# Kernel optimization log

Hardware: AMD Instinct MI355X
Metric: run time of the kernel (lower is better)

Reference implementation:

```python
import jax, jax.numpy as jnp
import numpy as np

N, M, DX, DY, H = 1024, 1024, 64, 16, 128
EPS = 1e-07


def setup_inputs() -> dict:
    key = jax.random.key(0)
    ks = jax.random.split(key, 9)
    din = DX + DY
    # Inputs
    X = jax.random.normal(ks[0], (N, DX), dtype=jnp.float32)
    U = jax.random.normal(ks[1], (M, DY), dtype=jnp.float32)
    Y = jax.random.normal(ks[2], (N, DY), dtype=jnp.float32)
    # MLP params (Linear(din,H), Softplus, Linear(H,H), Softplus, Linear(H,1))
    W1 = jax.random.normal(ks[3], (din, H), dtype=jnp.float32) / np.sqrt(din)
    b1 = jax.random.normal(ks[4], (H,), dtype=jnp.float32) * 0.01
    W2 = jax.random.normal(ks[5], (H, H), dtype=jnp.float32) / np.sqrt(H)
    b2 = jax.random.normal(ks[6], (H,), dtype=jnp.float32) * 0.01
    W3 = jax.random.normal(ks[7], (H, 1), dtype=jnp.float32) / np.sqrt(H)
    b3 = jax.random.normal(ks[8], (1,), dtype=jnp.float32) * 0.01
    return {"X_tensor": X, "U_tensor": U, "Y_tensor": Y,
            "W1": W1, "b1": b1, "W2": W2, "b2": b2, "W3": W3, "b3": b3}


def reference(X_tensor, U_tensor, Y_tensor, W1, b1, W2, b2, W3, b3):
    # phi_potential_network evaluated on every (x_i, u_j) pair.
    # Instead of materializing the [n, m, d_x + d_y] concatenation, split the
    # first linear layer: cat(x, u) @ W1 == x @ W1[:DX] + u @ W1[DX:]  (same math).
    hx = jnp.einsum('nd,dh->nh', X_tensor, W1[:DX])        # [n, H]
    hu = jnp.einsum('md,dh->mh', U_tensor, W1[DX:])        # [m, H]
    h = jax.nn.softplus(hx[:, None, :] + hu[None, :, :] + b1)   # [n, m, H]
    h = jax.nn.softplus(jnp.einsum('nmh,hk->nmk', h, W2) + b2)  # [n, m, H]
    phi_vals = jnp.einsum('nmh,hk->nmk', h, W3)[..., 0] + b3[0]  # [n, m]
    # entropic OT dual slackness + stable log-mean-exp over dual samples
    cost_matrix = Y_tensor @ U_tensor.T                     # [n, m]
    slackness = (cost_matrix - phi_vals) / EPS
    log_mean_exp = (jax.nn.logsumexp(slackness, axis=1, keepdims=True)
                    - jnp.log(jnp.float32(M)))
    psi_estimate = EPS * log_mean_exp                       # [n, 1]
    return psi_estimate
```

## Files before the change

kernel.cpp:

```cpp
#include <hip/hip_runtime.h>
#include <hip/hip_bf16.h>

#define NN 1024
#define MM 1024
#define DX 64
#define DY 16
#define HH 128

#define EPSF   1e-7f
#define LOG2E  1.4426950408889634f
#define LN2    0.6931471805599453f
#define K2     14426950.408889634f
#define LNM    6.9314718055994531f

typedef __bf16          bf16x8_t __attribute__((ext_vector_type(8)));
typedef float           f32x4_t  __attribute__((ext_vector_type(4)));
typedef unsigned short  u16x8_t  __attribute__((ext_vector_type(8)));

__device__ __forceinline__ unsigned short f2bf(float f) {
    unsigned int u = __float_as_uint(f);
    u += 0x7fffu + ((u >> 16) & 1u);
    return (unsigned short)(u >> 16);
}

__device__ __forceinline__ float sp(float x) {
    float t = __builtin_amdgcn_exp2f(x * LOG2E);
    return LN2 * __builtin_amdgcn_logf(1.0f + t);
}

__global__ void prep(const float* __restrict__ X, const float* __restrict__ U,
                     const float* __restrict__ Y, const float* __restrict__ W1,
                     const float* __restrict__ b1, const float* __restrict__ W2,
                     float* __restrict__ hx, float* __restrict__ hu,
                     unsigned short* __restrict__ w2t, float* __restrict__ costT)
{
    const int blk = blockIdx.x, tid = threadIdx.x;
    if (blk < NN) {
        const int n = blk, h = tid;
        float acc = b1[h];
        #pragma unroll 8
        for (int d = 0; d < DX; ++d) acc += X[n*DX+d] * W1[d*HH+h];
        hx[n*HH+h] = acc;
    } else if (blk < NN+MM) {
        const int m = blk - NN, h = tid;
        float acc = 0.f;
        #pragma unroll
        for (int d = 0; d < DY; ++d) acc += U[m*DY+d] * W1[(DX+d)*HH+h];
        hu[m*HH+h] = acc;
    } else if (blk < NN+MM+HH) {
        const int c = blk - (NN+MM), k = tid;
        w2t[c*HH+k] = f2bf(W2[k*HH+c]);
    } else {
        const int m = blk - (NN+MM+HH);
        float u[DY];
        #pragma unroll
        for (int d = 0; d < DY; ++d) u[d] = U[m*DY+d];
        #pragma unroll
        for (int r = 0; r < NN/128; ++r) {
            const int n = tid + r*128;
            float acc = 0.f;
            #pragma unroll
            for (int d = 0; d < DY; ++d) acc += Y[n*DY+d] * u[d];
            costT[m*NN+n] = acc;
        }
    }
}

__global__ __launch_bounds__(256, 2) void
otmain(const float* __restrict__ hx, const float* __restrict__ hu,
       const unsigned short* __restrict__ w2t,
       const float* __restrict__ b2, const float* __restrict__ W3,
       const float* __restrict__ b3, const float* __restrict__ costT,
       float* __restrict__ out)
{
    __shared__ unsigned short w2s[HH*HH];
    __shared__ float red[4][2][2];

    const int tid  = threadIdx.x;
    const int lane = tid & 63;
    const int w    = tid >> 6;
    const int nb   = blockIdx.x * 2;

    #pragma unroll
    for (int it = 0; it < 8; ++it) {
        const int chunk = tid + it*256;
        const int lin   = chunk << 4;
        const int c     = lin >> 8;
        const int swz   = lin ^ ((c & 7) << 4);
        *reinterpret_cast<u16x8_t*>(reinterpret_cast<char*>(w2s) + swz) =
            *reinterpret_cast<const u16x8_t*>(reinterpret_cast<const char*>(w2t) + lin);
    }

    const int il = lane & 1;
    const int jl = (lane >> 1) & 7;
    const int g  = lane >> 4;
    const int cl = lane & 15;

    float hxv[4][8];
    #pragma unroll
    for (int ks = 0; ks < 4; ++ks) {
        const float4 p0 = *reinterpret_cast<const float4*>(&hx[(nb+il)*HH + ks*32 + g*8]);
        const float4 p1 = *reinterpret_cast<const float4*>(&hx[(nb+il)*HH + ks*32 + g*8 + 4]);
        hxv[ks][0]=p0.x; hxv[ks][1]=p0.y; hxv[ks][2]=p0.z; hxv[ks][3]=p0.w;
        hxv[ks][4]=p1.x; hxv[ks][5]=p1.y; hxv[ks][6]=p1.z; hxv[ks][7]=p1.w;
    }
    float b2v[8], w3v[8];
    #pragma unroll
    for (int nt = 0; nt < 8; ++nt) { b2v[nt] = b2[nt*16+cl]; w3v[nt] = W3[nt*16+cl]; }
    const float b3v = b3[0];

    float mx[4], sv[4];
    #pragma unroll
    for (int q = 0; q < 4; ++q) { mx[q] = -3.0e38f; sv[q] = 0.f; }

    __syncthreads();

    for (int cch = 0; cch < 16; ++cch) {
        const int mb = cch * 64;
        const int m0 = mb + 16*w + jl;
        const int m1 = m0 + 8;
        f32x4_t acc0[8], acc1[8];
        #pragma unroll
        for (int nt = 0; nt < 8; ++nt)
            #pragma unroll
            for (int q = 0; q < 4; ++q) { acc0[nt][q] = 0.f; acc1[nt][q] = 0.f; }

        #pragma unroll
        for (int ks = 0; ks < 4; ++ks) {
            const int kf = ks*32 + g*8;
            const float4 u0a = *reinterpret_cast<const float4*>(&hu[m0*HH + kf]);
            const float4 u0b = *reinterpret_cast<const float4*>(&hu[m0*HH + kf + 4]);
            const float4 u1a = *reinterpret_cast<const float4*>(&hu[m1*HH + kf]);
            const float4 u1b = *reinterpret_cast<const float4*>(&hu[m1*HH + kf + 4]);
            u16x8_t a0u, a1u;
            a0u[0]=f2bf(sp(hxv[ks][0]+u0a.x)); a0u[1]=f2bf(sp(hxv[ks][1]+u0a.y));
            a0u[2]=f2bf(sp(hxv[ks][2]+u0a.z)); a0u[3]=f2bf(sp(hxv[ks][3]+u0a.w));
            a0u[4]=f2bf(sp(hxv[ks][4]+u0b.x)); a0u[5]=f2bf(sp(hxv[ks][5]+u0b.y));
            a0u[6]=f2bf(sp(hxv[ks][6]+u0b.z)); a0u[7]=f2bf(sp(hxv[ks][7]+u0b.w));
            a1u[0]=f2bf(sp(hxv[ks][0]+u1a.x)); a1u[1]=f2bf(sp(hxv[ks][1]+u1a.y));
            a1u[2]=f2bf(sp(hxv[ks][2]+u1a.z)); a1u[3]=f2bf(sp(hxv[ks][3]+u1a.w));
            a1u[4]=f2bf(sp(hxv[ks][4]+u1b.x)); a1u[5]=f2bf(sp(hxv[ks][5]+u1b.y));
            a1u[6]=f2bf(sp(hxv[ks][6]+u1b.z)); a1u[7]=f2bf(sp(hxv[ks][7]+u1b.w));
            const bf16x8_t a0 = __builtin_bit_cast(bf16x8_t, a0u);
            const bf16x8_t a1 = __builtin_bit_cast(bf16x8_t, a1u);

            #pragma unroll
            for (int nt = 0; nt < 8; ++nt) {
                const int cidx = nt*16 + cl;
                const int off  = (cidx*256 + ks*64 + g*16) ^ ((cidx & 7) << 4);
                const bf16x8_t bfr = *reinterpret_cast<const bf16x8_t*>(
                        reinterpret_cast<const char*>(w2s) + off);
                acc0[nt] = __builtin_amdgcn_mfma_f32_16x16x32_bf16(a0, bfr, acc0[nt], 0, 0, 0);
                acc1[nt] = __builtin_amdgcn_mfma_f32_16x16x32_bf16(a1, bfr, acc1[nt], 0, 0, 0);
            }
        }

        #pragma unroll
        for (int t = 0; t < 2; ++t) {
            float phi0=0.f, phi1=0.f, phi2=0.f, phi3=0.f;
            #pragma unroll
            for (int nt = 0; nt < 8; ++nt) {
                const f32x4_t a = t ? acc1[nt] : acc0[nt];
                phi0 += sp(a[0] + b2v[nt]) * w3v[nt];
                phi1 += sp(a[1] + b2v[nt]) * w3v[nt];
                phi2 += sp(a[2] + b2v[nt]) * w3v[nt];
                phi3 += sp(a[3] + b2v[nt]) * w3v[nt];
            }
            #pragma unroll
            for (int st = 1; st < 16; st <<= 1) {
                phi0 += __shfl_xor(phi0, st, 64);
                phi1 += __shfl_xor(phi1, st, 64);
                phi2 += __shfl_xor(phi2, st, 64);
                phi3 += __shfl_xor(phi3, st, 64);
            }
            const int jm = mb + 16*w + 8*t + 2*g;
            const float2 cA = *reinterpret_cast<const float2*>(&costT[jm*NN + nb]);
            const float2 cB = *reinterpret_cast<const float2*>(&costT[(jm+1)*NN + nb]);
            const float dv0 = cA.x - (phi0 + b3v);
            const float dv1 = cA.y - (phi1 + b3v);
            const float dv2 = cB.x - (phi2 + b3v);
            const float dv3 = cB.y - (phi3 + b3v);
            #define UPD(q, d) { const float mo = mx[q]; const float mn = fmaxf(mo, (d)); \
                sv[q] = sv[q]*__builtin_amdgcn_exp2f(K2*(mo-mn)) \
                      + __builtin_amdgcn_exp2f(K2*((d)-mn)); mx[q] = mn; }
            UPD(0, dv0) UPD(1, dv1) UPD(2, dv2) UPD(3, dv3)
            #undef UPD
        }
    }

    float fmx[2], fs[2];
    #pragma unroll
    for (int i = 0; i < 2; ++i) {
        const float m1v = mx[i], m2v = mx[i+2];
        const float Mv  = fmaxf(m1v, m2v);
        fmx[i] = Mv;
        fs[i]  = sv[i]  *__builtin_amdgcn_exp2f(K2*(m1v-Mv))
               + sv[i+2]*__builtin_amdgcn_exp2f(K2*(m2v-Mv));
    }
    if (cl != 0) { fs[0] = 0.f; fs[1] = 0.f; }
    #pragma unroll
    for (int st = 1; st < 64; st <<= 1) {
        #pragma unroll
        for (int i = 0; i < 2; ++i) {
            const float om = __shfl_xor(fmx[i], st, 64);
            const float os = __shfl_xor(fs[i],  st, 64);
            const float Mv = fmaxf(fmx[i], om);
            fs[i]  = fs[i]*__builtin_amdgcn_exp2f(K2*(fmx[i]-Mv))
                   + os  *__builtin_amdgcn_exp2f(K2*(om-Mv));
            fmx[i] = Mv;
        }
    }
    if (lane == 0) {
        red[w][0][0] = fmx[0]; red[w][0][1] = fs[0];
        red[w][1][0] = fmx[1]; red[w][1][1] = fs[1];
    }
    __syncthreads();
    if (tid < 2) {
        float Mv = red[0][tid][0], Sv = red[0][tid][1];
        #pragma unroll
        for (int ww = 1; ww < 4; ++ww) {
            const float om = red[ww][tid][0], os = red[ww][tid][1];
            const float M2 = fmaxf(Mv, om);
            Sv = Sv*__builtin_amdgcn_exp2f(K2*(Mv-M2))
               + os*__builtin_amdgcn_exp2f(K2*(om-M2));
            Mv = M2;
        }
        out[nb + tid] = Mv + EPSF*(LN2*__builtin_amdgcn_logf(Sv) - LNM);
    }
}

extern "C" void kernel_launch(void* const* d_in, const int* in_sizes, int n_in,
                              void* d_out, int out_size, void* d_ws, size_t ws_size,
                              hipStream_t stream)
{
    const float* X  = (const float*)d_in[0];
    const float* U  = (const float*)d_in[1];
    const float* Y  = (const float*)d_in[2];
    const float* W1 = (const float*)d_in[3];
    const float* b1 = (const float*)d_in[4];
    const float* W2 = (const float*)d_in[5];
    const float* b2 = (const float*)d_in[6];
    const float* W3 = (const float*)d_in[7];
    const float* b3 = (const float*)d_in[8];
    float* out = (float*)d_out;

    char* ws = (char*)d_ws;
    float*          hx    = (float*)(ws);
    float*          hu    = (float*)(ws + 524288);
    unsigned short* w2t   = (unsigned short*)(ws + 1048576);
    float*          costT = (float*)(ws + 1081344);

    prep<<<dim3(3200), dim3(128), 0, stream>>>(X, U, Y, W1, b1, W2, hx, hu, w2t, costT);
    otmain<<<dim3(512), dim3(256), 0, stream>>>(hx, hu, w2t, b2, W3, b3, costT, out);
}
```

Before: 206.4 us.

## Split m-range across two blocks per row pair, fold softplus constants, add merge kernel

The main kernel now launches twice as many blocks, each handling half of the m range, and writes partial (max, sum) pairs that a new merge kernel combines into the final log-mean-exp. The LOG2E/LN2 factors of softplus are folded into hx, hu, b2 and W3 in prep, and the online logsumexp update now uses a single exp2 per element. Launch bounds are raised to 4 blocks per CU, and the cost matrix is stored n-major so reads follow m. This is meant to fill more CUs and cut transcendental and multiply work, at the cost of an extra kernel launch, a workspace round-trip, and register pressure under the tighter launch bound.

After: 411.8 us. 2x slower.

```diff
diff --git a/kernel.cpp b/kernel.cpp
--- a/kernel.cpp
+++ b/kernel.cpp
@@ -23,16 +23,15 @@
     return (unsigned short)(u >> 16);
 }
 
-__device__ __forceinline__ float sp(float x) {
-    float t = __builtin_amdgcn_exp2f(x * LOG2E);
-    return LN2 * __builtin_amdgcn_logf(1.0f + t);
+__device__ __forceinline__ float l2e1(float s) {
+    return __builtin_amdgcn_logf(1.0f + __builtin_amdgcn_exp2f(s));
 }
 
 __global__ void prep(const float* __restrict__ X, const float* __restrict__ U,
                      const float* __restrict__ Y, const float* __restrict__ W1,
                      const float* __restrict__ b1, const float* __restrict__ W2,
                      float* __restrict__ hx, float* __restrict__ hu,
-                     unsigned short* __restrict__ w2t, float* __restrict__ costT)
+                     unsigned short* __restrict__ w2t, float* __restrict__ costN)
 {
     const int blk = blockIdx.x, tid = threadIdx.x;
     if (blk < NN) {
@@ -40,38 +39,38 @@
         float acc = b1[h];
         #pragma unroll 8
         for (int d = 0; d < DX; ++d) acc += X[n*DX+d] * W1[d*HH+h];
-        hx[n*HH+h] = acc;
+        hx[n*HH+h] = acc * LOG2E;
     } else if (blk < NN+MM) {
         const int m = blk - NN, h = tid;
         float acc = 0.f;
         #pragma unroll
         for (int d = 0; d < DY; ++d) acc += U[m*DY+d] * W1[(DX+d)*HH+h];
-        hu[m*HH+h] = acc;
+        hu[m*HH+h] = acc * LOG2E;
     } else if (blk < NN+MM+HH) {
         const int c = blk - (NN+MM), k = tid;
         w2t[c*HH+k] = f2bf(W2[k*HH+c]);
     } else {
-        const int m = blk - (NN+MM+HH);
-        float u[DY];
-        #pragma unroll
-        for (int d = 0; d < DY; ++d) u[d] = U[m*DY+d];
-        #pragma unroll
-        for (int r = 0; r < NN/128; ++r) {
-            const int n = tid + r*128;
+        const int n = blk - (NN+MM+HH);
+        float yv[DY];
+        #pragma unroll
+        for (int d = 0; d < DY; ++d) yv[d] = Y[n*DY+d];
+        #pragma unroll
+        for (int r = 0; r < MM/128; ++r) {
+            const int m = tid + r*128;
             float acc = 0.f;
             #pragma unroll
-            for (int d = 0; d < DY; ++d) acc += Y[n*DY+d] * u[d];
-            costT[m*NN+n] = acc;
-        }
-    }
-}
-
-__global__ __launch_bounds__(256, 2) void
+            for (int d = 0; d < DY; ++d) acc += U[m*DY+d] * yv[d];
+            costN[n*MM+m] = acc;
+        }
+    }
+}
+
+__global__ __launch_bounds__(256, 4) void
 otmain(const float* __restrict__ hx, const float* __restrict__ hu,
        const unsigned short* __restrict__ w2t,
        const float* __restrict__ b2, const float* __restrict__ W3,
-       const float* __restrict__ b3, const float* __restrict__ costT,
-       float* __restrict__ out)
+       const float* __restrict__ b3, const float* __restrict__ costN,
+       float2* __restrict__ part)
 {
     __shared__ unsigned short w2s[HH*HH];
     __shared__ float red[4][2][2];
@@ -79,7 +78,8 @@
     const int tid  = threadIdx.x;
     const int lane = tid & 63;
     const int w    = tid >> 6;
-    const int nb   = blockIdx.x * 2;
+    const int nb   = (blockIdx.x >> 1) * 2;
+    const int half = blockIdx.x & 1;
 
     #pragma unroll
     for (int it = 0; it < 8; ++it) {
@@ -106,7 +106,10 @@
     }
     float b2v[8], w3v[8];
     #pragma unroll
-    for (int nt = 0; nt < 8; ++nt) { b2v[nt] = b2[nt*16+cl]; w3v[nt] = W3[nt*16+cl]; }
+    for (int nt = 0; nt < 8; ++nt) {
+        b2v[nt] = b2[nt*16+cl] * LOG2E;
+        w3v[nt] = W3[nt*16+cl] * LN2;
+    }
     const float b3v = b3[0];
 
     float mx[4], sv[4];
@@ -115,8 +118,8 @@
 
     __syncthreads();
 
-    for (int cch = 0; cch < 16; ++cch) {
-        const int mb = cch * 64;
+    for (int cc = 0; cc < 8; ++cc) {
+        const int mb = (half*8 + cc) * 64;
         const int m0 = mb + 16*w + jl;
         const int m1 = m0 + 8;
         f32x4_t acc0[8], acc1[8];
@@ -132,17 +135,15 @@
             const float4 u0b = *reinterpret_cast<const float4*>(&hu[m0*HH + kf + 4]);
             const float4 u1a = *reinterpret_cast<const float4*>(&hu[m1*HH + kf]);
             const float4 u1b = *reinterpret_cast<const float4*>(&hu[m1*HH + kf + 4]);
-            u16x8_t a0u, a1u;
-            a0u[0]=f2bf(sp(hxv[ks][0]+u0a.x)); a0u[1]=f2bf(sp(hxv[ks][1]+u0a.y));
-            a0u[2]=f2bf(sp(hxv[ks][2]+u0a.z)); a0u[3]=f2bf(sp(hxv[ks][3]+u0a.w));
-            a0u[4]=f2bf(sp(hxv[ks][4]+u0b.x)); a0u[5]=f2bf(sp(hxv[ks][5]+u0b.y));
-            a0u[6]=f2bf(sp(hxv[ks][6]+u0b.z)); a0u[7]=f2bf(sp(hxv[ks][7]+u0b.w));
-            a1u[0]=f2bf(sp(hxv[ks][0]+u1a.x)); a1u[1]=f2bf(sp(hxv[ks][1]+u1a.y));
-            a1u[2]=f2bf(sp(hxv[ks][2]+u1a.z)); a1u[3]=f2bf(sp(hxv[ks][3]+u1a.w));
-            a1u[4]=f2bf(sp(hxv[ks][4]+u1b.x)); a1u[5]=f2bf(sp(hxv[ks][5]+u1b.y));
-            a1u[6]=f2bf(sp(hxv[ks][6]+u1b.z)); a1u[7]=f2bf(sp(hxv[ks][7]+u1b.w));
-            const bf16x8_t a0 = __builtin_bit_cast(bf16x8_t, a0u);
-            const bf16x8_t a1 = __builtin_bit_cast(bf16x8_t, a1u);
+            bf16x8_t a0, a1;
+            a0[0]=(__bf16)l2e1(hxv[ks][0]+u0a.x); a0[1]=(__bf16)l2e1(hxv[ks][1]+u0a.y);
+            a0[2]=(__bf16)l2e1(hxv[ks][2]+u0a.z); a0[3]=(__bf16)l2e1(hxv[ks][3]+u0a.w);
+            a0[4]=(__bf16)l2e1(hxv[ks][4]+u0b.x); a0[5]=(__bf16)l2e1(hxv[ks][5]+u0b.y);
+            a0[6]=(__bf16)l2e1(hxv[ks][6]+u0b.z); a0[7]=(__bf16)l2e1(hxv[ks][7]+u0b.w);
+            a1[0]=(__bf16)l2e1(hxv[ks][0]+u1a.x); a1[1]=(__bf16)l2e1(hxv[ks][1]+u1a.y);
+            a1[2]=(__bf16)l2e1(hxv[ks][2]+u1a.z); a1[3]=(__bf16)l2e1(hxv[ks][3]+u1a.w);
+            a1[4]=(__bf16)l2e1(hxv[ks][4]+u1b.x); a1[5]=(__bf16)l2e1(hxv[ks][5]+u1b.y);
+            a1[6]=(__bf16)l2e1(hxv[ks][6]+u1b.z); a1[7]=(__bf16)l2e1(hxv[ks][7]+u1b.w);
 
             #pragma unroll
             for (int nt = 0; nt < 8; ++nt) {
@@ -161,10 +162,10 @@
             #pragma unroll
             for (int nt = 0; nt < 8; ++nt) {
                 const f32x4_t a = t ? acc1[nt] : acc0[nt];
-                phi0 += sp(a[0] + b2v[nt]) * w3v[nt];
-                phi1 += sp(a[1] + b2v[nt]) * w3v[nt];
-                phi2 += sp(a[2] + b2v[nt]) * w3v[nt];
-                phi3 += sp(a[3] + b2v[nt]) * w3v[nt];
+                phi0 += l2e1(a[0] + b2v[nt]) * w3v[nt];
+                phi1 += l2e1(a[1] + b2v[nt]) * w3v[nt];
+                phi2 += l2e1(a[2] + b2v[nt]) * w3v[nt];
+                phi3 += l2e1(a[3] + b2v[nt]) * w3v[nt];
             }
             #pragma unroll
             for (int st = 1; st < 16; st <<= 1) {
@@ -174,15 +175,15 @@
                 phi3 += __shfl_xor(phi3, st, 64);
             }
             const int jm = mb + 16*w + 8*t + 2*g;
-            const float2 cA = *reinterpret_cast<const float2*>(&costT[jm*NN + nb]);
-            const float2 cB = *reinterpret_cast<const float2*>(&costT[(jm+1)*NN + nb]);
-            const float dv0 = cA.x - (phi0 + b3v);
-            const float dv1 = cA.y - (phi1 + b3v);
-            const float dv2 = cB.x - (phi2 + b3v);
-            const float dv3 = cB.y - (phi3 + b3v);
+            const float2 c0 = *reinterpret_cast<const float2*>(&costN[nb*MM + jm]);
+            const float2 c1 = *reinterpret_cast<const float2*>(&costN[(nb+1)*MM + jm]);
+            const float dv0 = c0.x - (phi0 + b3v);
+            const float dv1 = c1.x - (phi1 + b3v);
+            const float dv2 = c0.y - (phi2 + b3v);
+            const float dv3 = c1.y - (phi3 + b3v);
             #define UPD(q, d) { const float mo = mx[q]; const float mn = fmaxf(mo, (d)); \
-                sv[q] = sv[q]*__builtin_amdgcn_exp2f(K2*(mo-mn)) \
-                      + __builtin_amdgcn_exp2f(K2*((d)-mn)); mx[q] = mn; }
+                const float e = __builtin_amdgcn_exp2f(K2*(fminf(mo,(d))-mn)); \
+                sv[q] = ((d) <= mo) ? (sv[q] + e) : (sv[q]*e + 1.f); mx[q] = mn; }
             UPD(0, dv0) UPD(1, dv1) UPD(2, dv2) UPD(3, dv3)
             #undef UPD
         }
@@ -225,8 +226,19 @@
                + os*__builtin_amdgcn_exp2f(K2*(om-M2));
             Mv = M2;
         }
-        out[nb + tid] = Mv + EPSF*(LN2*__builtin_amdgcn_logf(Sv) - LNM);
-    }
+        part[(nb + tid)*2 + half] = make_float2(Mv, Sv);
+    }
+}
+
+__global__ void merge(const float2* __restrict__ part, float* __restrict__ out)
+{
+    const int n = blockIdx.x*256 + threadIdx.x;
+    if (n >= NN) return;
+    const float2 p0 = part[n*2+0], p1 = part[n*2+1];
+    const float M = fmaxf(p0.x, p1.x);
+    const float S = p0.y*__builtin_amdgcn_exp2f(K2*(p0.x-M))
+                  + p1.y*__builtin_amdgcn_exp2f(K2*(p1.x-M));
+    out[n] = M + EPSF*(LN2*__builtin_amdgcn_logf(S) - LNM);
 }
 
 extern "C" void kernel_launch(void* const* d_in, const int* in_sizes, int n_in,
@@ -248,8 +260,10 @@
     float*          hx    = (float*)(ws);
     float*          hu    = (float*)(ws + 524288);
     unsigned short* w2t   = (unsigned short*)(ws + 1048576);
-    float*          costT = (float*)(ws + 1081344);
-
-    prep<<<dim3(3200), dim3(128), 0, stream>>>(X, U, Y, W1, b1, W2, hx, hu, w2t, costT);
-    otmain<<<dim3(512), dim3(256), 0, stream>>>(hx, hu, w2t, b2, W3, b3, costT, out);
-}
+    float*          costN = (float*)(ws + 1081344);
+    float2*         part  = (float2*)(ws + 5275648);
+
+    prep<<<dim3(3200), dim3(128), 0, stream>>>(X, U, Y, W1, b1, W2, hx, hu, w2t, costN);
+    otmain<<<dim3(1024), dim3(256), 0, stream>>>(hx, hu, w2t, b2, W3, b3, costN, part);
+    merge<<<dim3(4), dim3(256), 0, stream>>>(part, out);
+}
```
